# Kernel optimization log

Measured on AMD Instinct MI355X. Metric: run time of the kernel, lower is better.

Reference implementation:

```python
import jax, jax.numpy as jnp
import numpy as np

D_MODEL = 1024
HEADS = 16
D_K = D_MODEL // HEADS
B, S = 2, 2048
NEG = -1e9


def setup_inputs() -> dict:
    key = jax.random.key(0)
    ks = jax.random.split(key, 12)
    sc = 1.0 / np.sqrt(D_MODEL)
    inp = {
        'query': jax.random.normal(ks[0], (B, S, D_MODEL), jnp.float32),
        'key': jax.random.normal(ks[1], (B, S, D_MODEL), jnp.float32),
        'value': jax.random.normal(ks[2], (B, S, D_MODEL), jnp.float32),
        'mask': jnp.tril(jnp.ones((S, S), jnp.int32))[None, None],  # [1,1,S,S] causal
        'Wq': jax.random.normal(ks[3], (D_MODEL, D_MODEL), jnp.float32) * sc,
        'bq': jax.random.normal(ks[4], (D_MODEL,), jnp.float32) * 0.02,
        'Wk': jax.random.normal(ks[5], (D_MODEL, D_MODEL), jnp.float32) * sc,
        'bk': jax.random.normal(ks[6], (D_MODEL,), jnp.float32) * 0.02,
        'Wv': jax.random.normal(ks[7], (D_MODEL, D_MODEL), jnp.float32) * sc,
        'bv': jax.random.normal(ks[8], (D_MODEL,), jnp.float32) * 0.02,
        'Wo': jax.random.normal(ks[9], (D_MODEL, D_MODEL), jnp.float32) * sc,
        'bo': jax.random.normal(ks[10], (D_MODEL,), jnp.float32) * 0.02,
    }
    return inp


def reference(query, key, value, mask, Wq, bq, Wk, bk, Wv, bv, Wo, bo):
    # QKV projections (torch Linear: x @ W.T + b; here W stored as [in,out])
    def split_heads(x):  # [B,S,D] -> [B,H,S,dk]
        return x.reshape(B, S, HEADS, D_K).transpose(0, 2, 1, 3)

    q = split_heads(query @ Wq + bq)
    k = split_heads(key @ Wk + bk)
    v = split_heads(value @ Wv + bv)

    scores = jnp.einsum('bhqd,bhkd->bhqk', q, k) / np.sqrt(D_K)
    scores = jnp.where(mask == 0, NEG, scores)
    attn = jax.nn.softmax(scores, axis=-1)  # dropout p=0 (eval) -> identity
    out = jnp.einsum('bhqk,bhkd->bhqd', attn, v)
    out = out.transpose(0, 2, 1, 3).reshape(B, S, D_MODEL)
    return out @ Wo + bo
```

## Files before the change

### kernel.cpp

```cpp
#include <hip/hip_runtime.h>
#include <hip/hip_bf16.h>
#include <cstdint>
#include <cstddef>

typedef short short8 __attribute__((ext_vector_type(8)));
typedef float f32x4 __attribute__((ext_vector_type(4)));
typedef float f32x16 __attribute__((ext_vector_type(16)));

#define SS 2048
#define DK 64
#define LAMBDA 0.18033688011112042f

__device__ __forceinline__ float b2f(ushort u) {
    union { uint32_t i; float f; } x; x.i = ((uint32_t)u) << 16; return x.f;
}
__device__ __forceinline__ ushort f2b(float f) {
    union { float f; uint32_t i; } x; x.f = f;
    uint32_t r = (x.i + 0x7fffu + ((x.i >> 16) & 1u)) >> 16;
    return (ushort)r;
}
__device__ __forceinline__ uint32_t pk_bf16(float a, float b) {
    union { __hip_bfloat162 v; uint32_t u; } x;
    float2 f2; f2.x = a; f2.y = b;
    x.v = __float22bfloat162_rn(f2);
    return x.u;
}

__device__ __forceinline__ void gl_lds16(const ushort* __restrict__ g, ushort* l) {
    __builtin_amdgcn_global_load_lds(
        (const __attribute__((address_space(1))) uint32_t*)(uintptr_t)g,
        (__attribute__((address_space(3))) uint32_t*)(uintptr_t)l, 16, 0, 0);
}

__device__ __forceinline__ bool probe_bf16(const uint32_t* __restrict__ probe) {
    const int lane = threadIdx.x & 63;
    int c = 0;
#pragma unroll
    for (int i = 0; i < 4; ++i) {
        uint32_t u = probe[lane * 4 + i];
        uint32_t e = (u >> 7) & 0xffu;
        c += (e >= 100u && e <= 140u) ? 1 : 0;
    }
    unsigned long long b = __ballot(c >= 3);
    return __popcll(b) > 32;
}

__device__ __forceinline__ void ld8_f32_to_bf16(ushort* dst, const float* __restrict__ src) {
    float4 a = *(const float4*)src;
    float4 b = *(const float4*)(src + 4);
    ushort t[8] = {f2b(a.x), f2b(a.y), f2b(a.z), f2b(a.w),
                   f2b(b.x), f2b(b.y), f2b(b.z), f2b(b.w)};
    *(uint4*)dst = *(uint4*)t;
}

__global__ __launch_bounds__(256) void transpose_all(const void* __restrict__ W0,
                                                     const void* __restrict__ W1,
                                                     const void* __restrict__ W2,
                                                     const void* __restrict__ W3,
                                                     ushort* __restrict__ ws,
                                                     const uint32_t* __restrict__ probe,
                                                     size_t wotOff) {
    __shared__ __align__(16) ushort t[64 * 72];
    const bool isbf = probe_bf16(probe);
    const int z = blockIdx.z;
    const void* W = (z == 0) ? W0 : (z == 1) ? W1 : (z == 2) ? W2 : W3;
    ushort* T = ws + ((z < 3) ? ((size_t)z << 20) : wotOff);

    const int n0 = blockIdx.x * 64, k0 = blockIdx.y * 64;
    const int tid = threadIdx.x;
    const int r = tid >> 3, cg = (tid & 7) * 8;
    if (isbf) {
        const ushort* Wb = (const ushort*)W;
#pragma unroll
        for (int p = 0; p < 2; ++p) {
            int k = r + p * 32;
            *(uint4*)&t[k * 72 + cg] = *(const uint4*)&Wb[(size_t)(k0 + k) * 1024 + n0 + cg];
        }
    } else {
        const float* Wf = (const float*)W;
#pragma unroll
        for (int p = 0; p < 2; ++p) {
            int k = r + p * 32;
            ld8_f32_to_bf16(&t[k * 72 + cg], &Wf[(size_t)(k0 + k) * 1024 + n0 + cg]);
        }
    }
    __syncthreads();
#pragma unroll
    for (int p = 0; p < 2; ++p) {
        int n = r + p * 32;
        uint4 o;
        ushort* op = (ushort*)&o;
#pragma unroll
        for (int i = 0; i < 8; ++i) op[i] = t[(cg + i) * 72 + n];
        *(uint4*)&T[(size_t)(n0 + n) * 1024 + k0 + cg] = o;
    }
}

__global__ __launch_bounds__(256) void conv_qkv(const void* __restrict__ q,
                                                const void* __restrict__ k,
                                                const void* __restrict__ v,
                                                ushort* __restrict__ ws,
                                                const uint32_t* __restrict__ probe,
                                                size_t dstOff) {
    const bool isbf = probe_bf16(probe);
    const int z = blockIdx.y;
    const void* src = (z == 0) ? q : (z == 1) ? k : v;
    ushort* dst = ws + dstOff + ((size_t)z << 22);
    const size_t i = ((size_t)blockIdx.x * 256 + threadIdx.x) * 8;
    if (isbf)
        *(uint4*)&dst[i] = *(const uint4*)&((const ushort*)src)[i];
    else
        ld8_f32_to_bf16(&dst[i], &((const float*)src)[i]);
}

template <int PRE>
__global__ __launch_bounds__(256, 3) void qkv_gemm(const void* __restrict__ qp,
                                                   const void* __restrict__ kp,
                                                   const void* __restrict__ vp,
                                                   const void* __restrict__ bqp,
                                                   const void* __restrict__ bkp,
                                                   const void* __restrict__ bvp,
                                                   ushort* __restrict__ ws,
                                                   const uint32_t* __restrict__ probe) {
    __shared__ __align__(16) ushort As[3][128 * 32];
    __shared__ __align__(16) ushort Bs[3][128 * 32];
    const bool isbf = probe_bf16(probe);
    const int z = blockIdx.z;
    const ushort* Bt = ws + ((size_t)z << 20);
    const void* bias = (z == 0) ? bqp : (z == 1) ? bkp : bvp;
    ushort* C = ws + ((size_t)((PRE ? 16 : 5) + 4 * z) << 20);
    const float scl = (z == 0) ? LAMBDA : 1.0f;

    const int tid = threadIdx.x;
    const int lane = tid & 63, wid = tid >> 6;
    const int l15 = lane & 15, g = lane >> 4;
    const int wm = wid >> 1, wn = wid & 1;
    const int id0 = blockIdx.y * 8 + blockIdx.x;
    const int id = (id0 & 7) * 32 + (id0 >> 3);
    const int m0 = (id >> 3) * 128, n0 = (id & 7) * 128;
    const int sr = tid >> 2, sc = (tid & 3) * 8;
    const int lrow = (lane >> 2), lcol = (lane & 3) * 8;

    f32x4 acc[4][4];
#pragma unroll
    for (int i = 0; i < 4; ++i)
#pragma unroll
        for (int j = 0; j < 4; ++j) {
            f32x4 zz = {0.f, 0.f, 0.f, 0.f};
            acc[i][j] = zz;
        }

    if (PRE) {
        const ushort* Ab = ws + ((size_t)(4 + 4 * z) << 20);
        auto stage1 = [&](int kk, int bsel) {
#pragma unroll
            for (int q = 0; q < 2; ++q) {
                const int row = (wid * 2 + q) * 16 + lrow;
                gl_lds16(&Bt[(size_t)(n0 + row) * 1024 + kk + lcol],
                         &Bs[bsel][(wid * 2 + q) * 512]);
                gl_lds16(&Ab[(size_t)(m0 + row) * 1024 + kk + lcol],
                         &As[bsel][(wid * 2 + q) * 512]);
            }
        };
        stage1(0, 0);
        stage1(32, 1);
        asm volatile("s_waitcnt vmcnt(4)" ::: "memory");
        __builtin_amdgcn_s_barrier();
        __builtin_amdgcn_sched_barrier(0);
        int cur = 0;
#pragma unroll 1
        for (int kk = 0; kk < 1024; kk += 32) {
            const int nxt = (cur >= 1) ? cur - 1 : cur + 2;
            if (kk + 64 < 1024) stage1(kk + 64, nxt);
            short8 a[4], b[4];
#pragma unroll
            for (int i = 0; i < 4; ++i)
                a[i] = *(const short8*)&As[cur][(wm * 64 + i * 16 + l15) * 32 + g * 8];
#pragma unroll
            for (int j = 0; j < 4; ++j)
                b[j] = *(const short8*)&Bs[cur][(wn * 64 + j * 16 + l15) * 32 + g * 8];
#pragma unroll
            for (int i = 0; i < 4; ++i)
#pragma unroll
                for (int j = 0; j < 4; ++j)
                    acc[i][j] =
                        __builtin_amdgcn_mfma_f32_16x16x32_bf16(a[i], b[j], acc[i][j], 0, 0, 0);
            if (kk + 32 < 1024) {
                if (kk + 64 < 1024)
                    asm volatile("s_waitcnt vmcnt(4)" ::: "memory");
                else
                    asm volatile("s_waitcnt vmcnt(0)" ::: "memory");
                __builtin_amdgcn_s_barrier();
                __builtin_amdgcn_sched_barrier(0);
            }
            cur = (cur == 2) ? 0 : cur + 1;
        }
    } else {
        auto stageAB = [&](int kk, int bsel) {
#pragma unroll
            for (int q = 0; q < 2; ++q) {
                const int row = (wid * 2 + q) * 16 + lrow;
                gl_lds16(&Bt[(size_t)(n0 + row) * 1024 + kk + lcol],
                         &Bs[bsel][(wid * 2 + q) * 512]);
            }
            const void* A = (z == 0) ? qp : (z == 1) ? kp : vp;
            if (isbf) {
                const ushort* Ab = (const ushort*)A;
#pragma unroll
                for (int q = 0; q < 2; ++q) {
                    const int row = (wid * 2 + q) * 16 + lrow;
                    gl_lds16(&Ab[(size_t)(m0 + row) * 1024 + kk + lcol],
                             &As[bsel][(wid * 2 + q) * 512]);
                }
            } else {
                const float* Af = (const float*)A;
                ld8_f32_to_bf16(&As[bsel][sr * 32 + sc], &Af[(size_t)(m0 + sr) * 1024 + kk + sc]);
                ld8_f32_to_bf16(&As[bsel][(sr + 64) * 32 + sc],
                                &Af[(size_t)(m0 + sr + 64) * 1024 + kk + sc]);
            }
        };
        stageAB(0, 0);
        __syncthreads();
#pragma unroll 2
        for (int kk = 0; kk < 1024; kk += 32) {
            const int cur = (kk >> 5) & 1;
            if (kk < 1024 - 32) stageAB(kk + 32, cur ^ 1);
            short8 a[4], b[4];
#pragma unroll
            for (int i = 0; i < 4; ++i)
                a[i] = *(const short8*)&As[cur][(wm * 64 + i * 16 + l15) * 32 + g * 8];
#pragma unroll
            for (int j = 0; j < 4; ++j)
                b[j] = *(const short8*)&Bs[cur][(wn * 64 + j * 16 + l15) * 32 + g * 8];
#pragma unroll
            for (int i = 0; i < 4; ++i)
#pragma unroll
                for (int j = 0; j < 4; ++j)
                    acc[i][j] =
                        __builtin_amdgcn_mfma_f32_16x16x32_bf16(a[i], b[j], acc[i][j], 0, 0, 0);
            __syncthreads();
        }
    }

#pragma unroll
    for (int i = 0; i < 4; ++i)
#pragma unroll
        for (int j = 0; j < 4; ++j) {
            const int col = n0 + wn * 64 + j * 16 + l15;
            const float bv = isbf ? b2f(((const ushort*)bias)[col]) : ((const float*)bias)[col];
#pragma unroll
            for (int r = 0; r < 4; ++r) {
                const int row = m0 + wm * 64 + i * 16 + g * 4 + r;
                const float v = (acc[i][j][r] + bv) * scl;
                size_t idx;
                if (z != 2) {
                    idx = ((size_t)((row >> 11) * 16 + (col >> 6)) * SS + (row & 2047)) * 64 +
                          (col & 63);
                } else {
                    idx = ((size_t)((row >> 11) * 16 + (col >> 6)) * 64 + (col & 63)) * SS +
                          (row & 2047);
                }
                C[idx] = f2b(v);
            }
        }
}

__global__ __launch_bounds__(256) void out_gemm(const ushort* __restrict__ A,
                                                const ushort* __restrict__ Bt,
                                                const void* __restrict__ bias,
                                                void* __restrict__ C,
                                                const uint32_t* __restrict__ probe) {
    __shared__ __align__(16) ushort As[3][64 * 32];
    __shared__ __align__(16) ushort Bs[3][128 * 32];
    const bool isbf = probe_bf16(probe);
    const int tid = threadIdx.x;
    const int lane = tid & 63, wid = tid >> 6;
    const int l15 = lane & 15, g = lane >> 4;
    const int wm = wid >> 1, wn = wid & 1;
    const int id0 = blockIdx.y * 8 + blockIdx.x;
    const int id = (id0 & 7) * 64 + (id0 >> 3);
    const int m0 = (id >> 3) * 64, n0 = (id & 7) * 128;
    const int lrow = (lane >> 2), lcol = (lane & 3) * 8;

    f32x4 acc[2][4];
#pragma unroll
    for (int i = 0; i < 2; ++i)
#pragma unroll
        for (int j = 0; j < 4; ++j) {
            f32x4 zz = {0.f, 0.f, 0.f, 0.f};
            acc[i][j] = zz;
        }

    auto stage1 = [&](int kk, int bsel) {
        {
            const int row = wid * 16 + lrow;
            gl_lds16(&A[(size_t)(m0 + row) * 1024 + kk + lcol], &As[bsel][wid * 512]);
        }
#pragma unroll
        for (int q = 0; q < 2; ++q) {
            const int row = (wid * 2 + q) * 16 + lrow;
            gl_lds16(&Bt[(size_t)(n0 + row) * 1024 + kk + lcol], &Bs[bsel][(wid * 2 + q) * 512]);
        }
    };

    stage1(0, 0);
    stage1(32, 1);
    asm volatile("s_waitcnt vmcnt(3)" ::: "memory");
    __builtin_amdgcn_s_barrier();
    __builtin_amdgcn_sched_barrier(0);
    int cur = 0;
#pragma unroll 1
    for (int kk = 0; kk < 1024; kk += 32) {
        const int nxt = (cur >= 1) ? cur - 1 : cur + 2;
        if (kk + 64 < 1024) stage1(kk + 64, nxt);
        short8 a[2], b[4];
#pragma unroll
        for (int i = 0; i < 2; ++i)
            a[i] = *(const short8*)&As[cur][(wm * 32 + i * 16 + l15) * 32 + g * 8];
#pragma unroll
        for (int j = 0; j < 4; ++j)
            b[j] = *(const short8*)&Bs[cur][(wn * 64 + j * 16 + l15) * 32 + g * 8];
#pragma unroll
        for (int i = 0; i < 2; ++i)
#pragma unroll
            for (int j = 0; j < 4; ++j)
                acc[i][j] = __builtin_amdgcn_mfma_f32_16x16x32_bf16(a[i], b[j], acc[i][j], 0, 0, 0);
        if (kk + 32 < 1024) {
            if (kk + 64 < 1024)
                asm volatile("s_waitcnt vmcnt(3)" ::: "memory");
            else
                asm volatile("s_waitcnt vmcnt(0)" ::: "memory");
            __builtin_amdgcn_s_barrier();
            __builtin_amdgcn_sched_barrier(0);
        }
        cur = (cur == 2) ? 0 : cur + 1;
    }

#pragma unroll
    for (int i = 0; i < 2; ++i)
#pragma unroll
        for (int j = 0; j < 4; ++j) {
            const int col = n0 + wn * 64 + j * 16 + l15;
            const float bv = isbf ? b2f(((const ushort*)bias)[col]) : ((const float*)bias)[col];
#pragma unroll
            for (int r = 0; r < 4; ++r) {
                const int row = m0 + wm * 32 + i * 16 + g * 4 + r;
                const float v = acc[i][j][r] + bv;
                const size_t idx = (size_t)row * 1024 + col;
                if (isbf)
                    ((ushort*)C)[idx] = f2b(v);
                else
                    ((float*)C)[idx] = v;
            }
        }
}

__global__ __launch_bounds__(256, 2) void attn_fwd(const ushort* __restrict__ Q,
                                                   const ushort* __restrict__ K,
                                                   const ushort* __restrict__ Vt,
                                                   ushort* __restrict__ O) {
    __shared__ __align__(16) ushort Ks[2][64 * 64];
    __shared__ __align__(16) ushort Vs[2][64 * 64];

    const int y = blockIdx.y;
    const int s0i = (blockIdx.x + y) & 15;
    const int t = (y & 16) ? (15 - s0i) : s0i;
    const int tid = threadIdx.x;
    const int lane = tid & 63, wid = tid >> 6;
    const int l31 = lane & 31, h = lane >> 5;

    const ushort* Qb = Q + (size_t)y * SS * DK;
    const ushort* Kb = K + (size_t)y * SS * DK;
    const ushort* Vb = Vt + (size_t)y * DK * SS;
    const int b = y >> 4, hh = y & 15;

    const int q0w = t * 128 + wid * 32;
    const int nkt = 2 * t + 2;

    const int srow = lane >> 3;
    const int sgc = ((lane & 7) ^ srow) * 8;

    short8 qf[4];
#pragma unroll
    for (int k4 = 0; k4 < 4; ++k4)
        qf[k4] = *(const short8*)&Qb[(size_t)(q0w + l31) * 64 + k4 * 16 + h * 8];

    int foff[2][4];
#pragma unroll
    for (int aa = 0; aa < 2; ++aa)
#pragma unroll
        for (int k4 = 0; k4 < 4; ++k4)
            foff[aa][k4] = (aa * 32 + l31) * 64 + (((k4 * 2 + h) ^ (l31 & 7)) * 8);

    f32x16 acc[2];
#pragma unroll
    for (int nt = 0; nt < 2; ++nt)
#pragma unroll
        for (int r = 0; r < 16; ++r) acc[nt][r] = 0.f;
    float lpA = 0.f, lpB = 0.f;

#pragma unroll
    for (int i = 0; i < 2; ++i) {
        const int chunk = wid * 2 + i;
        const int row = chunk * 8 + srow;
        gl_lds16(&Kb[(size_t)row * 64 + sgc], &Ks[0][chunk * 512]);
        gl_lds16(&Vb[(size_t)row * SS + sgc], &Vs[0][chunk * 512]);
    }
    __syncthreads();

#pragma unroll 1
    for (int kt = 0; kt < nkt; ++kt) {
        const int cur = kt & 1;
        if (kt + 1 < nkt) {
            const int k0n = (kt + 1) * 64;
#pragma unroll
            for (int i = 0; i < 2; ++i) {
                const int chunk = wid * 2 + i;
                const int row = chunk * 8 + srow;
                gl_lds16(&Kb[(size_t)(k0n + row) * 64 + sgc], &Ks[cur ^ 1][chunk * 512]);
                gl_lds16(&Vb[(size_t)row * SS + k0n + sgc], &Vs[cur ^ 1][chunk * 512]);
            }
        }

        if (q0w + 31 >= kt * 64) {
            f32x16 sc[2];
#pragma unroll
            for (int st = 0; st < 2; ++st)
#pragma unroll
                for (int r = 0; r < 16; ++r) sc[st][r] = 0.f;
#pragma unroll
            for (int st = 0; st < 2; ++st)
#pragma unroll
                for (int k4 = 0; k4 < 4; ++k4) {
                    short8 kb = *(const short8*)&Ks[cur][foff[st][k4]];
                    sc[st] = __builtin_amdgcn_mfma_f32_32x32x16_bf16(kb, qf[k4], sc[st], 0, 0, 0);
                }

            if (kt >= nkt - 2) {
                const int qg = q0w + l31;
#pragma unroll
                for (int st = 0; st < 2; ++st)
#pragma unroll
                    for (int r = 0; r < 16; ++r) {
                        const int kvg = kt * 64 + st * 32 + (r & 3) + 8 * (r >> 2) + 4 * h;
                        if (kvg > qg) sc[st][r] = -1e9f;
                    }
            }

            uint32_t pk8[2][8];
#pragma unroll
            for (int st = 0; st < 2; ++st) {
                float ls = 0.f;
#pragma unroll
                for (int i = 0; i < 8; ++i) {
                    const float p0 = exp2f(sc[st][2 * i]);
                    const float p1 = exp2f(sc[st][2 * i + 1]);
                    ls += p0 + p1;
                    pk8[st][i] = pk_bf16(p0, p1);
                }
                if (st == 0) lpA += ls; else lpB += ls;
            }

#pragma unroll
            for (int st = 0; st < 2; ++st) {
                asm("v_permlane32_swap_b32 %0, %1" : "+v"(pk8[st][0]), "+v"(pk8[st][2]));
                asm("v_permlane32_swap_b32 %0, %1" : "+v"(pk8[st][1]), "+v"(pk8[st][3]));
                asm("v_permlane32_swap_b32 %0, %1" : "+v"(pk8[st][4]), "+v"(pk8[st][6]));
                asm("v_permlane32_swap_b32 %0, %1" : "+v"(pk8[st][5]), "+v"(pk8[st][7]));
            }

#pragma unroll
            for (int ktv = 0; ktv < 4; ++ktv) {
                union { uint32_t u[4]; short8 s; } pa;
#pragma unroll
                for (int w4 = 0; w4 < 4; ++w4) pa.u[w4] = pk8[ktv >> 1][(ktv & 1) * 4 + w4];
#pragma unroll
                for (int nt = 0; nt < 2; ++nt) {
                    short8 vb = *(const short8*)&Vs[cur][foff[nt][ktv]];
                    acc[nt] =
                        __builtin_amdgcn_mfma_f32_32x32x16_bf16(pa.s, vb, acc[nt], 0, 0, 0);
                }
            }
        }

        __syncthreads();
    }

    const float lp = lpA + lpB;
    const float lt = lp + __shfl_xor(lp, 32);
    const float inv = 1.0f / lt;
#pragma unroll
    for (int r = 0; r < 16; ++r) {
        const int qrow = (r & 3) + 8 * (r >> 2) + 4 * h;
        const float ivr = __shfl(inv, qrow);
        const int rowg = q0w + qrow;
#pragma unroll
        for (int nt = 0; nt < 2; ++nt) {
            const int col = hh * 64 + nt * 32 + l31;
            O[(size_t)(b * SS + rowg) * 1024 + col] = f2b(acc[nt][r] * ivr);
        }
    }
}

extern "C" void kernel_launch(void* const* d_in, const int* in_sizes, int n_in,
                              void* d_out, int out_size, void* d_ws, size_t ws_size,
                              hipStream_t stream) {
    const void* q = d_in[0];
    const void* k = d_in[1];
    const void* v = d_in[2];
    const void* Wq = d_in[4];
    const void* bq = d_in[5];
    const void* Wk = d_in[6];
    const void* bk = d_in[7];
    const void* Wv = d_in[8];
    const void* bv = d_in[9];
    const void* Wo = d_in[10];
    const void* bo = d_in[11];
    const uint32_t* probe = (const uint32_t*)d_in[0];

    ushort* ws = (ushort*)d_ws;
    const size_t M = (size_t)1 << 20;
    const bool pre = ws_size >= 28 * M * sizeof(ushort);

    if (pre) {
        transpose_all<<<dim3(16, 16, 4), 256, 0, stream>>>(Wq, Wk, Wv, Wo, ws, probe, 3 * M);
        conv_qkv<<<dim3(2048, 3), 256, 0, stream>>>(q, k, v, ws, probe, 4 * M);
        qkv_gemm<1><<<dim3(8, 32, 3), 256, 0, stream>>>(q, k, v, bq, bk, bv, ws, probe);
        attn_fwd<<<dim3(16, 32), 256, 0, stream>>>(ws + 16 * M, ws + 20 * M, ws + 24 * M,
                                                   ws + 4 * M);
        out_gemm<<<dim3(8, 64), 256, 0, stream>>>(ws + 4 * M, ws + 3 * M, bo, d_out, probe);
    } else {
        transpose_all<<<dim3(16, 16, 4), 256, 0, stream>>>(Wq, Wk, Wv, Wo, ws, probe, 4 * M);
        qkv_gemm<0><<<dim3(8, 32, 3), 256, 0, stream>>>(q, k, v, bq, bk, bv, ws, probe);
        attn_fwd<<<dim3(16, 32), 256, 0, stream>>>(ws + 5 * M, ws + 9 * M, ws + 13 * M, ws);
        out_gemm<<<dim3(8, 64), 256, 0, stream>>>(ws, ws + 4 * M, bo, d_out, probe);
    }
}
```

Measured before the change: 233.1 us.

## Triple-buffer attention K/V tiles with padded LDS and skip bf16 input copy

The attention kernel now keeps three K/V tile buffers instead of two and prefetches two tiles ahead. It replaces the full __syncthreads with targeted vmcnt waits plus an s_barrier. LDS chunks are padded to a stride of 528 elements, which changes the bank mapping. Separately, when inputs are already bf16, the conversion kernel exits early and the QKV GEMM reads the activations directly, removing a copy pass. The cost is extra LDS per block, which may reduce occupancy, and more delicate wait-count bookkeeping.

```diff
diff --git a/kernel.cpp b/kernel.cpp
--- a/kernel.cpp
+++ b/kernel.cpp
@@ -10,6 +10,8 @@
 #define SS 2048
 #define DK 64
 #define LAMBDA 0.18033688011112042f
+
+#define CH 528
 
 __device__ __forceinline__ float b2f(ushort u) {
     union { uint32_t i; float f; } x; x.i = ((uint32_t)u) << 16; return x.f;
@@ -103,14 +105,12 @@
                                                 const uint32_t* __restrict__ probe,
                                                 size_t dstOff) {
     const bool isbf = probe_bf16(probe);
+    if (isbf) return;
     const int z = blockIdx.y;
     const void* src = (z == 0) ? q : (z == 1) ? k : v;
     ushort* dst = ws + dstOff + ((size_t)z << 22);
     const size_t i = ((size_t)blockIdx.x * 256 + threadIdx.x) * 8;
-    if (isbf)
-        *(uint4*)&dst[i] = *(const uint4*)&((const ushort*)src)[i];
-    else
-        ld8_f32_to_bf16(&dst[i], &((const float*)src)[i]);
+    ld8_f32_to_bf16(&dst[i], &((const float*)src)[i]);
 }
 
 template <int PRE>
@@ -151,7 +151,8 @@
         }
 
     if (PRE) {
-        const ushort* Ab = ws + ((size_t)(4 + 4 * z) << 20);
+        const ushort* Ab = isbf ? (const ushort*)((z == 0) ? qp : (z == 1) ? kp : vp)
+                                : ws + ((size_t)(4 + 4 * z) << 20);
         auto stage1 = [&](int kk, int bsel) {
 #pragma unroll
             for (int q = 0; q < 2; ++q) {
@@ -359,8 +360,8 @@
                                                    const ushort* __restrict__ K,
                                                    const ushort* __restrict__ Vt,
                                                    ushort* __restrict__ O) {
-    __shared__ __align__(16) ushort Ks[2][64 * 64];
-    __shared__ __align__(16) ushort Vs[2][64 * 64];
+    __shared__ __align__(16) ushort Ks[3][8 * CH];
+    __shared__ __align__(16) ushort Vs[3][8 * CH];
 
     const int y = blockIdx.y;
     const int s0i = (blockIdx.x + y) & 15;
@@ -390,7 +391,8 @@
     for (int aa = 0; aa < 2; ++aa)
 #pragma unroll
         for (int k4 = 0; k4 < 4; ++k4)
-            foff[aa][k4] = (aa * 32 + l31) * 64 + (((k4 * 2 + h) ^ (l31 & 7)) * 8);
+            foff[aa][k4] = (aa * 4 + (l31 >> 3)) * CH + (l31 & 7) * 64 +
+                           (((k4 * 2 + h) ^ (l31 & 7)) * 8);
 
     f32x16 acc[2];
 #pragma unroll
@@ -399,27 +401,28 @@
         for (int r = 0; r < 16; ++r) acc[nt][r] = 0.f;
     float lpA = 0.f, lpB = 0.f;
 
-#pragma unroll
-    for (int i = 0; i < 2; ++i) {
-        const int chunk = wid * 2 + i;
-        const int row = chunk * 8 + srow;
-        gl_lds16(&Kb[(size_t)row * 64 + sgc], &Ks[0][chunk * 512]);
-        gl_lds16(&Vb[(size_t)row * SS + sgc], &Vs[0][chunk * 512]);
-    }
-    __syncthreads();
-
+    auto stageKV = [&](int kt, int bsel) {
+#pragma unroll
+        for (int i = 0; i < 2; ++i) {
+            const int chunk = wid * 2 + i;
+            const int row = chunk * 8 + srow;
+            gl_lds16(&Kb[(size_t)(kt * 64 + row) * 64 + sgc], &Ks[bsel][chunk * CH]);
+            gl_lds16(&Vb[(size_t)row * SS + kt * 64 + sgc], &Vs[bsel][chunk * CH]);
+        }
+    };
+
+    stageKV(0, 0);
+    stageKV(1, 1);
+    asm volatile("s_waitcnt vmcnt(4)" ::: "memory");
+    __builtin_amdgcn_s_barrier();
+    __builtin_amdgcn_sched_barrier(0);
+
+    int cur = 0;
 #pragma unroll 1
     for (int kt = 0; kt < nkt; ++kt) {
-        const int cur = kt & 1;
-        if (kt + 1 < nkt) {
-            const int k0n = (kt + 1) * 64;
-#pragma unroll
-            for (int i = 0; i < 2; ++i) {
-                const int chunk = wid * 2 + i;
-                const int row = chunk * 8 + srow;
-                gl_lds16(&Kb[(size_t)(k0n + row) * 64 + sgc], &Ks[cur ^ 1][chunk * 512]);
-                gl_lds16(&Vb[(size_t)row * SS + k0n + sgc], &Vs[cur ^ 1][chunk * 512]);
-            }
+        if (kt + 2 < nkt) {
+            const int nxt = (cur >= 1) ? cur - 1 : cur + 2;
+            stageKV(kt + 2, nxt);
         }
 
         if (q0w + 31 >= kt * 64) {
@@ -483,7 +486,15 @@
             }
         }
 
-        __syncthreads();
+        if (kt + 1 < nkt) {
+            if (kt + 2 < nkt)
+                asm volatile("s_waitcnt vmcnt(4)" ::: "memory");
+            else
+                asm volatile("s_waitcnt vmcnt(0)" ::: "memory");
+            __builtin_amdgcn_s_barrier();
+            __builtin_amdgcn_sched_barrier(0);
+        }
+        cur = (cur == 2) ? 0 : cur + 1;
     }
 
     const float lp = lpA + lpB;
```

New measurement: 234.4 us. No clear change (+0.6%).

## Split attention KV loop across two waves per 32-row query block

Applied to the files above, without the earlier changes.

Rewrites the attention kernel so each 128-thread block handles 32 query rows, with its two waves processing alternating KV tiles and combining partial outputs and row sums through shared memory. Blocks are scheduled longest-first for causal load balancing. Also skips the bf16 input conversion copy by reading bf16 inputs directly in the QKV GEMM. Per-wave loads are no longer double-buffered, so load latency is exposed unless occupancy hides it.

```diff
diff --git a/kernel.cpp b/kernel.cpp
--- a/kernel.cpp
+++ b/kernel.cpp
@@ -103,14 +103,12 @@
                                                 const uint32_t* __restrict__ probe,
                                                 size_t dstOff) {
     const bool isbf = probe_bf16(probe);
+    if (isbf) return;
     const int z = blockIdx.y;
     const void* src = (z == 0) ? q : (z == 1) ? k : v;
     ushort* dst = ws + dstOff + ((size_t)z << 22);
     const size_t i = ((size_t)blockIdx.x * 256 + threadIdx.x) * 8;
-    if (isbf)
-        *(uint4*)&dst[i] = *(const uint4*)&((const ushort*)src)[i];
-    else
-        ld8_f32_to_bf16(&dst[i], &((const float*)src)[i]);
+    ld8_f32_to_bf16(&dst[i], &((const float*)src)[i]);
 }
 
 template <int PRE>
@@ -151,7 +149,8 @@
         }
 
     if (PRE) {
-        const ushort* Ab = ws + ((size_t)(4 + 4 * z) << 20);
+        const ushort* Ab = isbf ? (const ushort*)((z == 0) ? qp : (z == 1) ? kp : vp)
+                                : ws + ((size_t)(4 + 4 * z) << 20);
         auto stage1 = [&](int kk, int bsel) {
 #pragma unroll
             for (int q = 0; q < 2; ++q) {
@@ -355,16 +354,15 @@
         }
 }
 
-__global__ __launch_bounds__(256, 2) void attn_fwd(const ushort* __restrict__ Q,
+__global__ __launch_bounds__(128, 4) void attn_fwd(const ushort* __restrict__ Q,
                                                    const ushort* __restrict__ K,
                                                    const ushort* __restrict__ Vt,
                                                    ushort* __restrict__ O) {
-    __shared__ __align__(16) ushort Ks[2][64 * 64];
-    __shared__ __align__(16) ushort Vs[2][64 * 64];
+    __shared__ __align__(16) ushort Ks[2][8 * 512];
+    __shared__ __align__(16) ushort Vs[2][8 * 512];
 
     const int y = blockIdx.y;
-    const int s0i = (blockIdx.x + y) & 15;
-    const int t = (y & 16) ? (15 - s0i) : s0i;
+    const int t32 = 63 - blockIdx.x;
     const int tid = threadIdx.x;
     const int lane = tid & 63, wid = tid >> 6;
     const int l31 = lane & 31, h = lane >> 5;
@@ -374,23 +372,17 @@
     const ushort* Vb = Vt + (size_t)y * DK * SS;
     const int b = y >> 4, hh = y & 15;
 
-    const int q0w = t * 128 + wid * 32;
-    const int nkt = 2 * t + 2;
-
-    const int srow = lane >> 3;
-    const int sgc = ((lane & 7) ^ srow) * 8;
+    const int q0 = t32 * 32;
+    const int nkt = t32 / 2 + 1;
 
     short8 qf[4];
 #pragma unroll
     for (int k4 = 0; k4 < 4; ++k4)
-        qf[k4] = *(const short8*)&Qb[(size_t)(q0w + l31) * 64 + k4 * 16 + h * 8];
-
-    int foff[2][4];
-#pragma unroll
-    for (int aa = 0; aa < 2; ++aa)
-#pragma unroll
-        for (int k4 = 0; k4 < 4; ++k4)
-            foff[aa][k4] = (aa * 32 + l31) * 64 + (((k4 * 2 + h) ^ (l31 & 7)) * 8);
+        qf[k4] = *(const short8*)&Qb[(size_t)(q0 + l31) * 64 + k4 * 16 + h * 8];
+
+    const ushort* kbase = Kb + (size_t)l31 * 64 + h * 8;
+    const ushort* vbase = Vb + (size_t)l31 * SS + h * 8;
+    const int lo8 = lane * 8;
 
     f32x16 acc[2];
 #pragma unroll
@@ -399,105 +391,109 @@
         for (int r = 0; r < 16; ++r) acc[nt][r] = 0.f;
     float lpA = 0.f, lpB = 0.f;
 
-#pragma unroll
-    for (int i = 0; i < 2; ++i) {
-        const int chunk = wid * 2 + i;
-        const int row = chunk * 8 + srow;
-        gl_lds16(&Kb[(size_t)row * 64 + sgc], &Ks[0][chunk * 512]);
-        gl_lds16(&Vb[(size_t)row * SS + sgc], &Vs[0][chunk * 512]);
+#pragma unroll 1
+    for (int kt = wid; kt < nkt; kt += 2) {
+        asm volatile("s_waitcnt lgkmcnt(0)" ::: "memory");
+        {
+            const ushort* kb = kbase + (size_t)kt * 4096;
+            const ushort* vb = vbase + kt * 64;
+#pragma unroll
+            for (int f = 0; f < 8; ++f) {
+                gl_lds16(kb + (f >> 2) * 2048 + (f & 3) * 16, &Ks[wid][f * 512]);
+                gl_lds16(vb + (size_t)(f >> 2) * 32 * SS + (f & 3) * 16, &Vs[wid][f * 512]);
+            }
+        }
+        asm volatile("s_waitcnt vmcnt(0)" ::: "memory");
+        __builtin_amdgcn_sched_barrier(0);
+
+        f32x16 sc[2];
+#pragma unroll
+        for (int st = 0; st < 2; ++st) {
+#pragma unroll
+            for (int r = 0; r < 16; ++r) sc[st][r] = 0.f;
+#pragma unroll
+            for (int k4 = 0; k4 < 4; ++k4) {
+                short8 kb = *(const short8*)&Ks[wid][(st * 4 + k4) * 512 + lo8];
+                sc[st] = __builtin_amdgcn_mfma_f32_32x32x16_bf16(kb, qf[k4], sc[st], 0, 0, 0);
+            }
+        }
+
+        if (kt == nkt - 1) {
+            const int qg = q0 + l31;
+#pragma unroll
+            for (int st = 0; st < 2; ++st)
+#pragma unroll
+                for (int r = 0; r < 16; ++r) {
+                    const int kvg = kt * 64 + st * 32 + (r & 3) + 8 * (r >> 2) + 4 * h;
+                    if (kvg > qg) sc[st][r] = -1e9f;
+                }
+        }
+
+        uint32_t pk8[2][8];
+#pragma unroll
+        for (int st = 0; st < 2; ++st) {
+            float ls = 0.f;
+#pragma unroll
+            for (int i = 0; i < 8; ++i) {
+                const float p0 = exp2f(sc[st][2 * i]);
+                const float p1 = exp2f(sc[st][2 * i + 1]);
+                ls += p0 + p1;
+                pk8[st][i] = pk_bf16(p0, p1);
+            }
+            if (st == 0) lpA += ls; else lpB += ls;
+        }
+
+#pragma unroll
+        for (int st = 0; st < 2; ++st) {
+            asm("v_permlane32_swap_b32 %0, %1" : "+v"(pk8[st][0]), "+v"(pk8[st][2]));
+            asm("v_permlane32_swap_b32 %0, %1" : "+v"(pk8[st][1]), "+v"(pk8[st][3]));
+            asm("v_permlane32_swap_b32 %0, %1" : "+v"(pk8[st][4]), "+v"(pk8[st][6]));
+            asm("v_permlane32_swap_b32 %0, %1" : "+v"(pk8[st][5]), "+v"(pk8[st][7]));
+        }
+
+#pragma unroll
+        for (int ktv = 0; ktv < 4; ++ktv) {
+            union { uint32_t u[4]; short8 s; } pa;
+#pragma unroll
+            for (int w4 = 0; w4 < 4; ++w4) pa.u[w4] = pk8[ktv >> 1][(ktv & 1) * 4 + w4];
+#pragma unroll
+            for (int nt = 0; nt < 2; ++nt) {
+                short8 vb = *(const short8*)&Vs[wid][(nt * 4 + ktv) * 512 + lo8];
+                acc[nt] = __builtin_amdgcn_mfma_f32_32x32x16_bf16(pa.s, vb, acc[nt], 0, 0, 0);
+            }
+        }
+    }
+
+    if (wid == 1) {
+        float* mo = (float*)&Ks[1][0];
+#pragma unroll
+        for (int nt = 0; nt < 2; ++nt)
+#pragma unroll
+            for (int r = 0; r < 16; ++r) mo[(nt * 16 + r) * 64 + lane] = acc[nt][r];
+        ((float*)&Vs[1][0])[lane] = lpA + lpB;
     }
     __syncthreads();
-
-#pragma unroll 1
-    for (int kt = 0; kt < nkt; ++kt) {
-        const int cur = kt & 1;
-        if (kt + 1 < nkt) {
-            const int k0n = (kt + 1) * 64;
-#pragma unroll
-            for (int i = 0; i < 2; ++i) {
-                const int chunk = wid * 2 + i;
-                const int row = chunk * 8 + srow;
-                gl_lds16(&Kb[(size_t)(k0n + row) * 64 + sgc], &Ks[cur ^ 1][chunk * 512]);
-                gl_lds16(&Vb[(size_t)row * SS + k0n + sgc], &Vs[cur ^ 1][chunk * 512]);
-            }
-        }
-
-        if (q0w + 31 >= kt * 64) {
-            f32x16 sc[2];
-#pragma unroll
-            for (int st = 0; st < 2; ++st)
-#pragma unroll
-                for (int r = 0; r < 16; ++r) sc[st][r] = 0.f;
-#pragma unroll
-            for (int st = 0; st < 2; ++st)
-#pragma unroll
-                for (int k4 = 0; k4 < 4; ++k4) {
-                    short8 kb = *(const short8*)&Ks[cur][foff[st][k4]];
-                    sc[st] = __builtin_amdgcn_mfma_f32_32x32x16_bf16(kb, qf[k4], sc[st], 0, 0, 0);
-                }
-
-            if (kt >= nkt - 2) {
-                const int qg = q0w + l31;
-#pragma unroll
-                for (int st = 0; st < 2; ++st)
-#pragma unroll
-                    for (int r = 0; r < 16; ++r) {
-                        const int kvg = kt * 64 + st * 32 + (r & 3) + 8 * (r >> 2) + 4 * h;
-                        if (kvg > qg) sc[st][r] = -1e9f;
-                    }
-            }
-
-            uint32_t pk8[2][8];
-#pragma unroll
-            for (int st = 0; st < 2; ++st) {
-                float ls = 0.f;
-#pragma unroll
-                for (int i = 0; i < 8; ++i) {
-                    const float p0 = exp2f(sc[st][2 * i]);
-                    const float p1 = exp2f(sc[st][2 * i + 1]);
-                    ls += p0 + p1;
-                    pk8[st][i] = pk_bf16(p0, p1);
-                }
-                if (st == 0) lpA += ls; else lpB += ls;
-            }
-
-#pragma unroll
-            for (int st = 0; st < 2; ++st) {
-                asm("v_permlane32_swap_b32 %0, %1" : "+v"(pk8[st][0]), "+v"(pk8[st][2]));
-                asm("v_permlane32_swap_b32 %0, %1" : "+v"(pk8[st][1]), "+v"(pk8[st][3]));
-                asm("v_permlane32_swap_b32 %0, %1" : "+v"(pk8[st][4]), "+v"(pk8[st][6]));
-                asm("v_permlane32_swap_b32 %0, %1" : "+v"(pk8[st][5]), "+v"(pk8[st][7]));
-            }
-
-#pragma unroll
-            for (int ktv = 0; ktv < 4; ++ktv) {
-                union { uint32_t u[4]; short8 s; } pa;
-#pragma unroll
-                for (int w4 = 0; w4 < 4; ++w4) pa.u[w4] = pk8[ktv >> 1][(ktv & 1) * 4 + w4];
-#pragma unroll
-                for (int nt = 0; nt < 2; ++nt) {
-                    short8 vb = *(const short8*)&Vs[cur][foff[nt][ktv]];
-                    acc[nt] =
-                        __builtin_amdgcn_mfma_f32_32x32x16_bf16(pa.s, vb, acc[nt], 0, 0, 0);
-                }
-            }
-        }
-
-        __syncthreads();
-    }
-
-    const float lp = lpA + lpB;
-    const float lt = lp + __shfl_xor(lp, 32);
-    const float inv = 1.0f / lt;
-#pragma unroll
-    for (int r = 0; r < 16; ++r) {
-        const int qrow = (r & 3) + 8 * (r >> 2) + 4 * h;
-        const float ivr = __shfl(inv, qrow);
-        const int rowg = q0w + qrow;
-#pragma unroll
-        for (int nt = 0; nt < 2; ++nt) {
-            const int col = hh * 64 + nt * 32 + l31;
-            O[(size_t)(b * SS + rowg) * 1024 + col] = f2b(acc[nt][r] * ivr);
+    if (wid == 0) {
+        const float* mo = (const float*)&Ks[1][0];
+        const float lp1 = ((const float*)&Vs[1][0])[lane];
+#pragma unroll
+        for (int nt = 0; nt < 2; ++nt)
+#pragma unroll
+            for (int r = 0; r < 16; ++r) acc[nt][r] += mo[(nt * 16 + r) * 64 + lane];
+
+        const float lp = lpA + lpB + lp1;
+        const float lt = lp + __shfl_xor(lp, 32);
+        const float inv = 1.0f / lt;
+#pragma unroll
+        for (int r = 0; r < 16; ++r) {
+            const int qrow = (r & 3) + 8 * (r >> 2) + 4 * h;
+            const float ivr = __shfl(inv, qrow);
+            const int rowg = q0 + qrow;
+#pragma unroll
+            for (int nt = 0; nt < 2; ++nt) {
+                const int col = hh * 64 + nt * 32 + l31;
+                O[(size_t)(b * SS + rowg) * 1024 + col] = f2b(acc[nt][r] * ivr);
+            }
         }
     }
 }
@@ -526,13 +522,13 @@
         transpose_all<<<dim3(16, 16, 4), 256, 0, stream>>>(Wq, Wk, Wv, Wo, ws, probe, 3 * M);
         conv_qkv<<<dim3(2048, 3), 256, 0, stream>>>(q, k, v, ws, probe, 4 * M);
         qkv_gemm<1><<<dim3(8, 32, 3), 256, 0, stream>>>(q, k, v, bq, bk, bv, ws, probe);
-        attn_fwd<<<dim3(16, 32), 256, 0, stream>>>(ws + 16 * M, ws + 20 * M, ws + 24 * M,
+        attn_fwd<<<dim3(64, 32), 128, 0, stream>>>(ws + 16 * M, ws + 20 * M, ws + 24 * M,
                                                    ws + 4 * M);
         out_gemm<<<dim3(8, 64), 256, 0, stream>>>(ws + 4 * M, ws + 3 * M, bo, d_out, probe);
     } else {
         transpose_all<<<dim3(16, 16, 4), 256, 0, stream>>>(Wq, Wk, Wv, Wo, ws, probe, 4 * M);
         qkv_gemm<0><<<dim3(8, 32, 3), 256, 0, stream>>>(q, k, v, bq, bk, bv, ws, probe);
-        attn_fwd<<<dim3(16, 32), 256, 0, stream>>>(ws + 5 * M, ws + 9 * M, ws + 13 * M, ws);
+        attn_fwd<<<dim3(64, 32), 128, 0, stream>>>(ws + 5 * M, ws + 9 * M, ws + 13 * M, ws);
         out_gemm<<<dim3(8, 64), 256, 0, stream>>>(ws, ws + 4 * M, bo, d_out, probe);
     }
 }
```

Result: slower. 306.5 us (+31.5%).
